# Kernel optimization log

Hardware: AMD Instinct MI355X
Metric: run time of the kernel (lower is better)

## Reference

```python
import jax, jax.numpy as jnp
import numpy as np

N = 100000      # total nodes
E = 800000      # directed edges
DIN = 256       # input feature dim
H = 128         # hidden dim
EPS = 1e-5      # BatchNorm eps


def setup_inputs() -> dict:
    key = jax.random.key(0)
    ks = jax.random.split(key, 18)
    s = 0.05
    return {
        "x": jax.random.normal(ks[0], (N, DIN), jnp.float32),
        "src": jax.random.randint(ks[1], (E,), 0, N, dtype=jnp.int32),
        "dst": jax.random.randint(ks[2], (E,), 0, N, dtype=jnp.int32),
        "W1": jax.random.normal(ks[3], (DIN, H), jnp.float32) * s,
        "b1": jnp.zeros((H,), jnp.float32),
        "g1": jnp.ones((H,), jnp.float32),
        "be1": jnp.zeros((H,), jnp.float32),
        "W2": jax.random.normal(ks[4], (H, H), jnp.float32) * s,
        "b2": jnp.zeros((H,), jnp.float32),
        "g2": jnp.ones((H,), jnp.float32),
        "be2": jnp.zeros((H,), jnp.float32),
        "W3": jax.random.normal(ks[5], (H, H), jnp.float32) * s,
        "b3": jnp.zeros((H,), jnp.float32),
        "g3": jnp.ones((H,), jnp.float32),
        "be3": jnp.zeros((H,), jnp.float32),
        "Wf": jax.random.normal(ks[6], (H, 1), jnp.float32) * s,
        "bf": jnp.zeros((1,), jnp.float32),
    }


def _gcn_conv(h, W, b, src, dst, dis):
    # GCNConv: project, then sym-normalized aggregation over edges + self-loops
    h = h @ W                                   # [N, out]
    coef = dis[src] * dis[dst]                  # [E] edge norm weights
    agg = jax.ops.segment_sum(h[src] * coef[:, None], dst, num_segments=N)
    agg = agg + h * (dis * dis)[:, None]        # self-loop term (norm = 1/deg)
    return agg + b


def _bn_relu(h, g, be):
    # BatchNorm1d in training mode (batch stats over nodes, biased variance)
    mu = jnp.mean(h, axis=0)
    var = jnp.var(h, axis=0)
    return jax.nn.relu((h - mu) * (g / jnp.sqrt(var + EPS)) + be)


def reference(x, src, dst, W1, b1, g1, be1, W2, b2, g2, be2,
              W3, b3, g3, be3, Wf, bf):
    # degree of (A + I) counted on destination nodes, edge weight 1
    deg = jax.ops.segment_sum(jnp.ones((E,), jnp.float32), dst, num_segments=N) + 1.0
    dis = jax.lax.rsqrt(deg)                    # deg >= 1, safe

    h = _bn_relu(_gcn_conv(x, W1, b1, src, dst, dis), g1, be1)
    h = _bn_relu(_gcn_conv(h, W2, b2, src, dst, dis), g2, be2)
    h = _bn_relu(_gcn_conv(h, W3, b3, src, dst, dis), g3, be3)
    return h @ Wf + bf                          # [N, 1]
```

## Files before the change

### kernel.cpp

```cpp
#include <hip/hip_runtime.h>
#include <hip/hip_bf16.h>

typedef unsigned short ushort_t;
typedef __bf16 bf16x8 __attribute__((ext_vector_type(8)));
typedef unsigned short ushort8 __attribute__((ext_vector_type(8)));
typedef unsigned short ushort4v __attribute__((ext_vector_type(4)));
typedef float f32x4 __attribute__((ext_vector_type(4)));

#define HH 128
#define EPS 1e-5f
#define STAT_SLICES 32
#define MM1_GRID 512
#define MMBN_GRID 1024

__device__ __forceinline__ float bf2f(ushort_t u) {
    unsigned v = ((unsigned)u) << 16;
    return __builtin_bit_cast(float, v);
}
__device__ __forceinline__ ushort_t f2bf(float f) {
    unsigned u = __builtin_bit_cast(unsigned, f);
    unsigned r = (u + 0x7fffu + ((u >> 16) & 1u)) >> 16;
    return (ushort_t)r;
}
__device__ __forceinline__ float cvt(const void* p, int i, int flag) {
    return flag ? bf2f(((const ushort_t*)p)[i]) : ((const float*)p)[i];
}

__global__ void preK(const int* __restrict__ dst, int* __restrict__ counts, int E,
                     const void* W1, ushort_t* Wt1, const void* W2, ushort_t* Wt2,
                     const void* W3, ushort_t* Wt3,
                     const void* g1, const void* b1, const void* b2, const void* b3,
                     const void* g2, const void* g3, const void* be1, const void* be2,
                     const void* be3, const void* Wfp, const void* bfp,
                     float* __restrict__ cvec, int histB) {
    const int bid = blockIdx.x;
    const int tid = threadIdx.x;
    const int flag = (((const ushort_t*)g1)[0] == 0x3F80) ? 1 : 0;
    if (bid < histB) {
        int e = bid * 256 + tid;
        if (e < E) atomicAdd(&counts[dst[e]], 1);
    } else if (bid < histB + 256) {
        int idx = (bid - histB) * 256 + tid;
        const void* W; ushort_t* Wt; int K;
        if (idx < 32768)      { W = W1; Wt = Wt1; K = 256; }
        else if (idx < 49152) { W = W2; Wt = Wt2; K = 128; idx -= 32768; }
        else                  { W = W3; Wt = Wt3; K = 128; idx -= 49152; }
        int k = idx >> 7, nn = idx & 127;
        Wt[nn * K + k] = flag ? ((const ushort_t*)W)[idx] : f2bf(((const float*)W)[idx]);
    } else {
        int t = tid;
        if (t < 128) {
            cvec[t]        = cvt(b1, t, flag);
            cvec[128 + t]  = cvt(b2, t, flag);
            cvec[256 + t]  = cvt(b3, t, flag);
            cvec[384 + t]  = cvt(g1, t, flag);
            cvec[512 + t]  = cvt(g2, t, flag);
            cvec[640 + t]  = cvt(g3, t, flag);
            cvec[768 + t]  = cvt(be1, t, flag);
            cvec[896 + t]  = cvt(be2, t, flag);
            cvec[1024 + t] = cvt(be3, t, flag);
            cvec[1152 + t] = cvt(Wfp, t, flag);
            if (t == 0) cvec[1280] = cvt(bfp, 0, flag);
        }
    }
}

__global__ void scanAdisK(const int* __restrict__ cnt, int* __restrict__ partial,
                          float* __restrict__ dis, int n, int nbScan) {
    __shared__ int lds[256];
    const int tid = threadIdx.x;
    if ((int)blockIdx.x < nbScan) {
        int base = blockIdx.x * 2048 + tid * 8;
        int s = 0;
#pragma unroll
        for (int j = 0; j < 8; ++j) { int idx = base + j; if (idx < n) s += cnt[idx]; }
        lds[tid] = s; __syncthreads();
        for (int off = 128; off; off >>= 1) { if (tid < off) lds[tid] += lds[tid + off]; __syncthreads(); }
        if (tid == 0) partial[blockIdx.x] = lds[0];
    } else {
        int i = (blockIdx.x - nbScan) * 256 + tid;
        if (i < n) dis[i] = rsqrtf((float)cnt[i] + 1.0f);
    }
}

__device__ __forceinline__ void scanC2Dev(int* lds, const int* __restrict__ cnt,
                                          const int* __restrict__ partial,
                                          int* __restrict__ rowptr, int n, int bid, int nb) {
    const int tid = threadIdx.x;
    int pre = 0, tot = 0;
    for (int i = 0; i < nb; ++i) { int v = partial[i]; if (i < bid) pre += v; tot += v; }
    int base = bid * 2048 + tid * 8;
    int v[8]; int s = 0;
#pragma unroll
    for (int j = 0; j < 8; ++j) { int idx = base + j; v[j] = (idx < n) ? cnt[idx] : 0; s += v[j]; }
    lds[tid] = s; __syncthreads();
    for (int off = 1; off < 256; off <<= 1) {
        int x = (tid >= off) ? lds[tid - off] : 0;
        __syncthreads();
        lds[tid] += x;
        __syncthreads();
    }
    int excl = lds[tid] - s;
    int off0 = pre + excl;
#pragma unroll
    for (int j = 0; j < 8; ++j) {
        int idx = base + j;
        if (idx < n) { rowptr[idx] = off0; off0 += v[j]; }
    }
    if (bid == 0 && tid == 0) rowptr[n] = tot;
}

__global__ void scatterK(const int* __restrict__ src, const int* __restrict__ dst,
                         const int* __restrict__ rowptr, int* __restrict__ fill,
                         const float* __restrict__ dis,
                         uint2* __restrict__ erec, int E) {
    int e = blockIdx.x * 256 + threadIdx.x;
    if (e >= E) return;
    int d = dst[e], s = src[e];
    int old = atomicSub(&fill[d], 1);
    int pos = rowptr[d] + old - 1;
    float c = dis[s] * dis[d];
    uint2 r; r.x = (unsigned)s; r.y = __builtin_bit_cast(unsigned, c);
    erec[pos] = r;
}

__global__ __launch_bounds__(256) void mm1scanCK(const void* __restrict__ x,
                                                 const ushort_t* __restrict__ Wt1,
                                                 ushort_t* __restrict__ tbuf, int n,
                                                 const ushort_t* __restrict__ flagRef,
                                                 const int* __restrict__ cnt,
                                                 const int* __restrict__ partial,
                                                 int* __restrict__ rowptr, int nbScan) {
    __shared__ char smem[65536];
    const int tid = threadIdx.x;
    if ((int)blockIdx.x < nbScan) {
        scanC2Dev((int*)smem, cnt, partial, rowptr, n, blockIdx.x, nbScan);
        return;
    }
    const int bid = blockIdx.x - nbScan;

#pragma unroll
    for (int it = 0; it < 16; ++it) {
        int idx = tid + it * 256;
        int row = idx >> 5, seg = idx & 31;
        int p = seg ^ (row & 7);
        *(uint4*)&smem[row * 512 + p * 16] = *(const uint4*)&Wt1[row * 256 + seg * 8];
    }
    __syncthreads();

    const int lane = tid & 63, wave = tid >> 6;
    const int m = lane & 15, q = lane >> 4;
    const int flag = (flagRef[0] == 0x3F80) ? 1 : 0;
    const int nTiles = (n + 63) >> 6;

    auto loadA = [&](int tile, ushort8* a) {
        int r = tile * 64 + wave * 16 + m;
        if (r >= n) r = n - 1;
        if (flag) {
            const ushort_t* p0 = (const ushort_t*)x + (size_t)r * 256 + q * 8;
#pragma unroll
            for (int s = 0; s < 8; ++s) a[s] = *(const ushort8*)(p0 + s * 32);
        } else {
            const float* p0 = (const float*)x + (size_t)r * 256 + q * 8;
#pragma unroll
            for (int s = 0; s < 8; ++s) {
                float4 f0 = *(const float4*)(p0 + s * 32);
                float4 f1 = *(const float4*)(p0 + s * 32 + 4);
                a[s][0] = f2bf(f0.x); a[s][1] = f2bf(f0.y); a[s][2] = f2bf(f0.z); a[s][3] = f2bf(f0.w);
                a[s][4] = f2bf(f1.x); a[s][5] = f2bf(f1.y); a[s][6] = f2bf(f1.z); a[s][7] = f2bf(f1.w);
            }
        }
    };

    ushort8 cur[8], nxt[8];
    int tile = bid;
    if (tile < nTiles) loadA(tile, cur);
    for (; tile < nTiles; tile += MM1_GRID) {
        int tnext = tile + MM1_GRID;
        if (tnext < nTiles) loadA(tnext, nxt);

        f32x4 acc[8];
#pragma unroll
        for (int t = 0; t < 8; ++t) acc[t] = (f32x4){0.f, 0.f, 0.f, 0.f};
#pragma unroll
        for (int s = 0; s < 8; ++s) {
            bf16x8 nf = __builtin_bit_cast(bf16x8, cur[s]);
#pragma unroll
            for (int t = 0; t < 8; ++t) {
                int p = (s * 4 + q) ^ (m & 7);
                ushort8 wv = *(const ushort8*)&smem[(t * 16 + m) * 512 + p * 16];
                acc[t] = __builtin_amdgcn_mfma_f32_16x16x32_bf16(
                    __builtin_bit_cast(bf16x8, wv), nf, acc[t], 0, 0, 0);
            }
        }
        int node_g = tile * 64 + wave * 16 + m;
        if (node_g < n) {
            ushort_t* op = tbuf + (size_t)node_g * HH + q * 4;
#pragma unroll
            for (int t = 0; t < 8; ++t) {
                ushort4v pk;
#pragma unroll
                for (int r = 0; r < 4; ++r) pk[r] = f2bf(acc[t][r]);
                *(ushort4v*)(op + t * 16) = pk;
            }
        }
#pragma unroll
        for (int s = 0; s < 8; ++s) cur[s] = nxt[s];
    }
}

__global__ __launch_bounds__(256) void mmBNK(const ushort_t* __restrict__ A,
                                             const ushort_t* __restrict__ Wt,
                                             ushort_t* __restrict__ out, int n,
                                             const float* __restrict__ ssum,
                                             const float* __restrict__ ssq,
                                             const float* __restrict__ gam,
                                             const float* __restrict__ bet) {
    __shared__ char smem[33792];
    float* scw = (float*)(smem + 32768);
    const int tid = threadIdx.x;

    if (tid < 128) {
        float S = 0.f, Q = 0.f;
#pragma unroll
        for (int sl = 0; sl < STAT_SLICES; ++sl) { S += ssum[sl * HH + tid]; Q += ssq[sl * HH + tid]; }
        float invn = 1.0f / (float)n;
        float mu = S * invn;
        float var = fmaxf(Q * invn - mu * mu, 0.f);
        float sc = gam[tid] * rsqrtf(var + EPS);
        scw[tid] = sc;
        scw[128 + tid] = bet[tid] - mu * sc;
    }
#pragma unroll
    for (int it = 0; it < 8; ++it) {
        int idx = tid + it * 256;
        int row = idx >> 4, seg = idx & 15;
        int p = seg ^ (row & 7);
        *(uint4*)&smem[row * 256 + p * 16] = *(const uint4*)&Wt[row * 128 + seg * 8];
    }
    __syncthreads();

    const int lane = tid & 63, wave = tid >> 6;
    const int m = lane & 15, q = lane >> 4;
    const int nTiles = (n + 63) >> 6;

    auto loadA = [&](int tile, ushort8* a) {
        int r = tile * 64 + wave * 16 + m;
        if (r >= n) r = n - 1;
        const ushort_t* p0 = A + (size_t)r * 128 + q * 8;
#pragma unroll
        for (int s = 0; s < 4; ++s) a[s] = *(const ushort8*)(p0 + s * 32);
    };

    ushort8 cur[4], nxt[4];
    int tile = blockIdx.x;
    if (tile < nTiles) loadA(tile, cur);
    for (; tile < nTiles; tile += MMBN_GRID) {
        int tnext = tile + MMBN_GRID;
        if (tnext < nTiles) loadA(tnext, nxt);

#pragma unroll
        for (int s = 0; s < 4; ++s) {
            int kb = s * 32 + q * 8;
#pragma unroll
            for (int j = 0; j < 8; ++j)
                cur[s][j] = f2bf(fmaxf(bf2f(cur[s][j]) * scw[kb + j] + scw[128 + kb + j], 0.f));
        }

        f32x4 acc[8];
#pragma unroll
        for (int t = 0; t < 8; ++t) acc[t] = (f32x4){0.f, 0.f, 0.f, 0.f};
#pragma unroll
        for (int s = 0; s < 4; ++s) {
            bf16x8 nf = __builtin_bit_cast(bf16x8, cur[s]);
#pragma unroll
            for (int t = 0; t < 8; ++t) {
                int p = (s * 4 + q) ^ (m & 7);
                ushort8 wv = *(const ushort8*)&smem[(t * 16 + m) * 256 + p * 16];
                acc[t] = __builtin_amdgcn_mfma_f32_16x16x32_bf16(
                    __builtin_bit_cast(bf16x8, wv), nf, acc[t], 0, 0, 0);
            }
        }
        int node_g = tile * 64 + wave * 16 + m;
        if (node_g < n) {
            ushort_t* op = out + (size_t)node_g * HH + q * 4;
#pragma unroll
            for (int t = 0; t < 8; ++t) {
                ushort4v pk;
#pragma unroll
                for (int r = 0; r < 4; ++r) pk[r] = f2bf(acc[t][r]);
                *(ushort4v*)(op + t * 16) = pk;
            }
        }
#pragma unroll
        for (int s = 0; s < 4; ++s) cur[s] = nxt[s];
    }
}

__global__ __launch_bounds__(256) void aggK(const ushort_t* __restrict__ t,
                                            const uint2* __restrict__ erec,
                                            const int* __restrict__ rowptr,
                                            const float* __restrict__ dis,
                                            const float* __restrict__ bias,
                                            ushort_t* __restrict__ g,
                                            float* __restrict__ ssum, float* __restrict__ ssq,
                                            int n) {
    const int lane = threadIdx.x & 63;
    const int wave = threadIdx.x >> 6;
    const int cb = lane * 2;
    const float b0 = bias[cb], b1 = bias[cb + 1];
    float s0 = 0.f, s1 = 0.f, q0 = 0.f, q1 = 0.f;

    for (int node = blockIdx.x * 4 + wave; node < n; node += gridDim.x * 4) {
        float d = dis[node];
        float d2 = d * d;
        unsigned sv = *(const unsigned*)(t + (size_t)node * HH + cb);
        float a0 = bf2f((ushort_t)(sv & 0xffff)) * d2;
        float a1 = bf2f((ushort_t)(sv >> 16)) * d2;

        int beg = rowptr[node], end = rowptr[node + 1];
        for (int eb = beg; eb < end; eb += 64) {
            int rem = end - eb; if (rem > 64) rem = 64;
            uint2 rec = (lane < rem) ? erec[eb + lane] : (uint2){0u, 0u};
            int es = (int)rec.x;
            float ec = __builtin_bit_cast(float, rec.y);
            int rr = (rem + 7) & ~7;
            for (int j = 0; j < rr; j += 8) {
                int ii[8]; float cc[8]; unsigned ww[8];
#pragma unroll
                for (int k = 0; k < 8; ++k) {
                    ii[k] = __shfl(es, j + k);
                    cc[k] = __shfl(ec, j + k);
                }
#pragma unroll
                for (int k = 0; k < 8; ++k)
                    ww[k] = *(const unsigned*)(t + (size_t)ii[k] * HH + cb);
#pragma unroll
                for (int k = 0; k < 8; ++k) {
                    a0 += bf2f((ushort_t)(ww[k] & 0xffff)) * cc[k];
                    a1 += bf2f((ushort_t)(ww[k] >> 16)) * cc[k];
                }
            }
        }
        a0 += b0; a1 += b1;
        unsigned packed = (unsigned)f2bf(a0) | ((unsigned)f2bf(a1) << 16);
        *(unsigned*)(g + (size_t)node * HH + cb) = packed;
        s0 += a0; s1 += a1; q0 += a0 * a0; q1 += a1 * a1;
    }

    __shared__ float red[4][64][4];
    red[wave][lane][0] = s0; red[wave][lane][1] = s1;
    red[wave][lane][2] = q0; red[wave][lane][3] = q1;
    __syncthreads();
    if (wave == 0) {
        float S0 = 0, S1 = 0, Q0 = 0, Q1 = 0;
#pragma unroll
        for (int w = 0; w < 4; ++w) {
            S0 += red[w][lane][0]; S1 += red[w][lane][1];
            Q0 += red[w][lane][2]; Q1 += red[w][lane][3];
        }
        int slice = (blockIdx.x & (STAT_SLICES - 1)) * HH;
        atomicAdd(&ssum[slice + cb], S0);
        atomicAdd(&ssum[slice + cb + 1], S1);
        atomicAdd(&ssq[slice + cb], Q0);
        atomicAdd(&ssq[slice + cb + 1], Q1);
    }
}

__global__ __launch_bounds__(256) void outK(const ushort_t* __restrict__ g,
                                            const float* __restrict__ ssum,
                                            const float* __restrict__ ssq,
                                            const float* __restrict__ gam,
                                            const float* __restrict__ bet,
                                            const float* __restrict__ Wf,
                                            const float* __restrict__ bfp,
                                            void* __restrict__ outv, int n,
                                            const ushort_t* __restrict__ flagRef) {
    __shared__ float scw[256];
    const int tid = threadIdx.x;
    if (tid < 128) {
        float S = 0.f, Q = 0.f;
#pragma unroll
        for (int sl = 0; sl < STAT_SLICES; ++sl) { S += ssum[sl * HH + tid]; Q += ssq[sl * HH + tid]; }
        float invn = 1.0f / (float)n;
        float mu = S * invn;
        float var = fmaxf(Q * invn - mu * mu, 0.f);
        float sc = gam[tid] * rsqrtf(var + EPS);
        scw[tid] = sc;
        scw[128 + tid] = bet[tid] - mu * sc;
    }
    __syncthreads();

    const int lane = tid & 63;
    const int wave = tid >> 6;
    const int cb = lane * 2;
    const float w0 = Wf[cb], w1 = Wf[cb + 1];
    const float sc0 = scw[cb], sc1 = scw[cb + 1];
    const float sh0 = scw[128 + cb], sh1 = scw[128 + cb + 1];
    const float bb = bfp[0];
    const int flag = (flagRef[0] == 0x3F80) ? 1 : 0;

    for (int node = blockIdx.x * 4 + wave; node < n; node += gridDim.x * 4) {
        unsigned v = *(const unsigned*)(g + (size_t)node * HH + cb);
        float h0 = fmaxf(bf2f((ushort_t)(v & 0xffff)) * sc0 + sh0, 0.f);
        float h1 = fmaxf(bf2f((ushort_t)(v >> 16)) * sc1 + sh1, 0.f);
        float x = h0 * w0 + h1 * w1;
#pragma unroll
        for (int off = 32; off; off >>= 1) x += __shfl_down(x, off);
        if (lane == 0) {
            float r = x + bb;
            if (flag) ((ushort_t*)outv)[node] = f2bf(r);
            else      ((float*)outv)[node] = r;
        }
    }
}

extern "C" void kernel_launch(void* const* d_in, const int* in_sizes, int n_in,
                              void* d_out, int out_size, void* d_ws, size_t ws_size,
                              hipStream_t stream) {
    const int DIN = 256;
    const int N = in_sizes[0] / DIN;
    const int E = in_sizes[1];

    const void* x   = d_in[0];
    const int*  src = (const int*)d_in[1];
    const int*  dst = (const int*)d_in[2];
    const void* W1  = d_in[3];
    const void* b1  = d_in[4];
    const void* g1  = d_in[5];
    const void* be1 = d_in[6];
    const void* W2  = d_in[7];
    const void* b2  = d_in[8];
    const void* g2  = d_in[9];
    const void* be2 = d_in[10];
    const void* W3  = d_in[11];
    const void* b3  = d_in[12];
    const void* g3  = d_in[13];
    const void* be3 = d_in[14];
    const void* Wf  = d_in[15];
    const void* bfp = d_in[16];
    const ushort_t* flagRef = (const ushort_t*)g1;

    char* base = (char*)d_ws;
    size_t off = 0;
    auto carve = [&](size_t bytes) -> void* {
        void* p = base + off;
        off += (bytes + 255) & ~(size_t)255;
        return p;
    };
    int*      counts = (int*)carve((size_t)N * 4);
    float*    stats  = (float*)carve((size_t)3 * 2 * STAT_SLICES * HH * 4);
    size_t    zbytes = off;
    float*    dis    = (float*)carve((size_t)N * 4);
    int*      rowptr = (int*)carve((size_t)(N + 1) * 4);
    int*      partial= (int*)carve(256 * 4);
    uint2*    erec   = (uint2*)carve((size_t)E * 8);
    ushort_t* Wt1    = (ushort_t*)carve((size_t)128 * 256 * 2);
    ushort_t* Wt2    = (ushort_t*)carve((size_t)128 * 128 * 2);
    ushort_t* Wt3    = (ushort_t*)carve((size_t)128 * 128 * 2);
    ushort_t* tbuf   = (ushort_t*)carve((size_t)N * HH * 2);
    ushort_t* gbuf   = (ushort_t*)carve((size_t)N * HH * 2);
    float*    cvec   = (float*)carve((size_t)1281 * 4);

    float* ssum0 = stats;                         float* ssq0 = ssum0 + STAT_SLICES * HH;
    float* ssum1 = ssq0 + STAT_SLICES * HH;       float* ssq1 = ssum1 + STAT_SLICES * HH;
    float* ssum2 = ssq1 + STAT_SLICES * HH;       float* ssq2 = ssum2 + STAT_SLICES * HH;

    float* c_b1 = cvec;         float* c_b2 = cvec + 128;  float* c_b3 = cvec + 256;
    float* c_g1 = cvec + 384;   float* c_g2 = cvec + 512;  float* c_g3 = cvec + 640;
    float* c_be1 = cvec + 768;  float* c_be2 = cvec + 896; float* c_be3 = cvec + 1024;
    float* c_Wf = cvec + 1152;  float* c_bf = cvec + 1280;

    const int nbScan = (N + 2047) / 2048;
    const int histB  = (E + 255) / 256;
    const int disB   = (N + 255) / 256;
    const int aggB   = 2048;

    hipMemsetAsync(d_ws, 0, zbytes, stream);

    preK<<<histB + 256 + 1, 256, 0, stream>>>(dst, counts, E, W1, Wt1, W2, Wt2, W3, Wt3,
                                              g1, b1, b2, b3, g2, g3, be1, be2, be3, Wf, bfp,
                                              cvec, histB);
    scanAdisK<<<nbScan + disB, 256, 0, stream>>>(counts, partial, dis, N, nbScan);
    mm1scanCK<<<nbScan + MM1_GRID, 256, 0, stream>>>(x, Wt1, tbuf, N, flagRef,
                                                     counts, partial, rowptr, nbScan);
    scatterK<<<histB, 256, 0, stream>>>(src, dst, rowptr, counts, dis, erec, E);

    aggK<<<aggB, 256, 0, stream>>>(tbuf, erec, rowptr, dis, c_b1, gbuf, ssum0, ssq0, N);
    mmBNK<<<MMBN_GRID, 256, 0, stream>>>(gbuf, Wt2, tbuf, N, ssum0, ssq0, c_g1, c_be1);
    aggK<<<aggB, 256, 0, stream>>>(tbuf, erec, rowptr, dis, c_b2, gbuf, ssum1, ssq1, N);
    mmBNK<<<MMBN_GRID, 256, 0, stream>>>(gbuf, Wt3, tbuf, N, ssum1, ssq1, c_g2, c_be2);
    aggK<<<aggB, 256, 0, stream>>>(tbuf, erec, rowptr, dis, c_b3, gbuf, ssum2, ssq2, N);
    outK<<<1024, 256, 0, stream>>>(gbuf, ssum2, ssq2, c_g3, c_be3, c_Wf, c_bf, d_out, N, flagRef);
}
```

Measured before the change: 452.9 us.

## Stage A tiles via global_load_lds DMA and split first GEMM output columns

Both GEMM kernels now copy the activation tile straight from global memory into LDS with global_load_lds, replacing register prefetch with double-buffered cur/nxt arrays. The first GEMM splits its 128 output columns into two halves across block pairs, so each block keeps half of W1 in LDS, and the fp32 input path converts rows into LDS. The mmBN grid shrinks from 1024 to 768. This removes the software prefetch overlap, so each tile waits for its DMA before the MFMAs run, and the column split makes each input tile be read twice from global memory.

```diff
diff --git a/kernel.cpp b/kernel.cpp
--- a/kernel.cpp
+++ b/kernel.cpp
@@ -10,8 +10,8 @@
 #define HH 128
 #define EPS 1e-5f
 #define STAT_SLICES 32
-#define MM1_GRID 512
-#define MMBN_GRID 1024
+#define GAS __attribute__((address_space(1)))
+#define LAS __attribute__((address_space(3)))
 
 __device__ __forceinline__ float bf2f(ushort_t u) {
     unsigned v = ((unsigned)u) << 16;
@@ -24,6 +24,9 @@
 }
 __device__ __forceinline__ float cvt(const void* p, int i, int flag) {
     return flag ? bf2f(((const ushort_t*)p)[i]) : ((const float*)p)[i];
+}
+__device__ __forceinline__ void dma16(const void* g, void* l) {
+    __builtin_amdgcn_global_load_lds((const GAS unsigned*)g, (LAS unsigned*)l, 16, 0, 0);
 }
 
 __global__ void preK(const int* __restrict__ dst, int* __restrict__ counts, int E,
@@ -134,17 +137,18 @@
     __shared__ char smem[65536];
     const int tid = threadIdx.x;
     if ((int)blockIdx.x < nbScan) {
-        scanC2Dev((int*)smem, cnt, partial, rowptr, n, blockIdx.x, nbScan);
+        scanC2Dev((int*)smem, cnt, partial, rowptr, n, blockIdx.x - 0, nbScan);
         return;
     }
-    const int bid = blockIdx.x - nbScan;
-
-#pragma unroll
-    for (int it = 0; it < 16; ++it) {
+    const int arm = blockIdx.x - nbScan;
+    const int ch  = arm & 1;
+
+#pragma unroll
+    for (int it = 0; it < 8; ++it) {
         int idx = tid + it * 256;
-        int row = idx >> 5, seg = idx & 31;
-        int p = seg ^ (row & 7);
-        *(uint4*)&smem[row * 512 + p * 16] = *(const uint4*)&Wt1[row * 256 + seg * 8];
+        int r = idx >> 5, seg = idx & 31;
+        int p = seg ^ (r & 7);
+        *(uint4*)&smem[r * 512 + p * 16] = *(const uint4*)&Wt1[(size_t)(ch * 64 + r) * 256 + seg * 8];
     }
     __syncthreads();
 
@@ -152,60 +156,62 @@
     const int m = lane & 15, q = lane >> 4;
     const int flag = (flagRef[0] == 0x3F80) ? 1 : 0;
     const int nTiles = (n + 63) >> 6;
-
-    auto loadA = [&](int tile, ushort8* a) {
-        int r = tile * 64 + wave * 16 + m;
-        if (r >= n) r = n - 1;
+    char* abuf = smem + 32768;
+
+    for (int tile = (arm >> 1); tile < nTiles; tile += 256) {
+        const int row0 = tile * 64 + wave * 16;
         if (flag) {
-            const ushort_t* p0 = (const ushort_t*)x + (size_t)r * 256 + q * 8;
-#pragma unroll
-            for (int s = 0; s < 8; ++s) a[s] = *(const ushort8*)(p0 + s * 32);
+#pragma unroll
+            for (int j = 0; j < 8; ++j) {
+                int r = row0 + j * 2;
+                if (r + 1 >= n) r = n - 2;
+                const char* g = (const char*)x + (size_t)r * 512 + lane * 16;
+                dma16(g, abuf + (wave * 16 + j * 2) * 512);
+            }
+            __builtin_amdgcn_s_waitcnt(0x0F70);
         } else {
-            const float* p0 = (const float*)x + (size_t)r * 256 + q * 8;
-#pragma unroll
-            for (int s = 0; s < 8; ++s) {
-                float4 f0 = *(const float4*)(p0 + s * 32);
-                float4 f1 = *(const float4*)(p0 + s * 32 + 4);
-                a[s][0] = f2bf(f0.x); a[s][1] = f2bf(f0.y); a[s][2] = f2bf(f0.z); a[s][3] = f2bf(f0.w);
-                a[s][4] = f2bf(f1.x); a[s][5] = f2bf(f1.y); a[s][6] = f2bf(f1.z); a[s][7] = f2bf(f1.w);
-            }
-        }
-    };
-
-    ushort8 cur[8], nxt[8];
-    int tile = bid;
-    if (tile < nTiles) loadA(tile, cur);
-    for (; tile < nTiles; tile += MM1_GRID) {
-        int tnext = tile + MM1_GRID;
-        if (tnext < nTiles) loadA(tnext, nxt);
-
-        f32x4 acc[8];
-#pragma unroll
-        for (int t = 0; t < 8; ++t) acc[t] = (f32x4){0.f, 0.f, 0.f, 0.f};
+#pragma unroll
+            for (int j = 0; j < 8; ++j) {
+                int r = row0 + j * 2;
+                if (r + 1 >= n) r = n - 2;
+                int rr = r + (lane >> 5);
+                int off = (lane & 31) * 8;
+                const float* p = (const float*)x + (size_t)rr * 256 + off;
+                float4 f0 = *(const float4*)p, f1 = *(const float4*)(p + 4);
+                ushort8 v;
+                v[0] = f2bf(f0.x); v[1] = f2bf(f0.y); v[2] = f2bf(f0.z); v[3] = f2bf(f0.w);
+                v[4] = f2bf(f1.x); v[5] = f2bf(f1.y); v[6] = f2bf(f1.z); v[7] = f2bf(f1.w);
+                *(ushort8*)&abuf[(wave * 16 + j * 2) * 512 + lane * 16] = v;
+            }
+        }
+
+        f32x4 acc[4];
+#pragma unroll
+        for (int t = 0; t < 4; ++t) acc[t] = (f32x4){0.f, 0.f, 0.f, 0.f};
+        const char* arow = abuf + (wave * 16 + m) * 512;
 #pragma unroll
         for (int s = 0; s < 8; ++s) {
-            bf16x8 nf = __builtin_bit_cast(bf16x8, cur[s]);
-#pragma unroll
-            for (int t = 0; t < 8; ++t) {
+            ushort8 av = *(const ushort8*)(arow + s * 64 + q * 16);
+            bf16x8 nf = __builtin_bit_cast(bf16x8, av);
+#pragma unroll
+            for (int t = 0; t < 4; ++t) {
                 int p = (s * 4 + q) ^ (m & 7);
                 ushort8 wv = *(const ushort8*)&smem[(t * 16 + m) * 512 + p * 16];
                 acc[t] = __builtin_amdgcn_mfma_f32_16x16x32_bf16(
                     __builtin_bit_cast(bf16x8, wv), nf, acc[t], 0, 0, 0);
             }
         }
-        int node_g = tile * 64 + wave * 16 + m;
-        if (node_g < n) {
-            ushort_t* op = tbuf + (size_t)node_g * HH + q * 4;
-#pragma unroll
-            for (int t = 0; t < 8; ++t) {
+        int node = tile * 64 + wave * 16 + m;
+        if (node < n) {
+            ushort_t* op = tbuf + (size_t)node * HH + ch * 64 + q * 4;
+#pragma unroll
+            for (int t = 0; t < 4; ++t) {
                 ushort4v pk;
 #pragma unroll
                 for (int r = 0; r < 4; ++r) pk[r] = f2bf(acc[t][r]);
                 *(ushort4v*)(op + t * 16) = pk;
             }
         }
-#pragma unroll
-        for (int s = 0; s < 8; ++s) cur[s] = nxt[s];
     }
 }
 
@@ -216,8 +222,9 @@
                                              const float* __restrict__ ssq,
                                              const float* __restrict__ gam,
                                              const float* __restrict__ bet) {
-    __shared__ char smem[33792];
-    float* scw = (float*)(smem + 32768);
+    __shared__ char smem[50176];
+    char* abuf = smem + 32768;
+    float* scw = (float*)(smem + 49152);
     const int tid = threadIdx.x;
 
     if (tid < 128) {
@@ -234,9 +241,9 @@
 #pragma unroll
     for (int it = 0; it < 8; ++it) {
         int idx = tid + it * 256;
-        int row = idx >> 4, seg = idx & 15;
-        int p = seg ^ (row & 7);
-        *(uint4*)&smem[row * 256 + p * 16] = *(const uint4*)&Wt[row * 128 + seg * 8];
+        int r = idx >> 4, seg = idx & 15;
+        int p = seg ^ (r & 7);
+        *(uint4*)&smem[r * 256 + p * 16] = *(const uint4*)&Wt[(size_t)r * 128 + seg * 8];
     }
     __syncthreads();
 
@@ -244,35 +251,29 @@
     const int m = lane & 15, q = lane >> 4;
     const int nTiles = (n + 63) >> 6;
 
-    auto loadA = [&](int tile, ushort8* a) {
-        int r = tile * 64 + wave * 16 + m;
-        if (r >= n) r = n - 1;
-        const ushort_t* p0 = A + (size_t)r * 128 + q * 8;
-#pragma unroll
-        for (int s = 0; s < 4; ++s) a[s] = *(const ushort8*)(p0 + s * 32);
-    };
-
-    ushort8 cur[4], nxt[4];
-    int tile = blockIdx.x;
-    if (tile < nTiles) loadA(tile, cur);
-    for (; tile < nTiles; tile += MMBN_GRID) {
-        int tnext = tile + MMBN_GRID;
-        if (tnext < nTiles) loadA(tnext, nxt);
-
+    for (int tile = blockIdx.x; tile < nTiles; tile += gridDim.x) {
+        const int row0 = tile * 64 + wave * 16;
+#pragma unroll
+        for (int j = 0; j < 4; ++j) {
+            int r = row0 + j * 4;
+            if (r + 3 >= n) r = n - 4;
+            const char* g = (const char*)A + (size_t)r * 256 + lane * 16;
+            dma16(g, abuf + (wave * 16 + j * 4) * 256);
+        }
+        __builtin_amdgcn_s_waitcnt(0x0F70);
+
+        f32x4 acc[8];
+#pragma unroll
+        for (int t = 0; t < 8; ++t) acc[t] = (f32x4){0.f, 0.f, 0.f, 0.f};
+        const char* arow = abuf + (wave * 16 + m) * 256;
 #pragma unroll
         for (int s = 0; s < 4; ++s) {
+            ushort8 av = *(const ushort8*)(arow + s * 64 + q * 16);
             int kb = s * 32 + q * 8;
 #pragma unroll
             for (int j = 0; j < 8; ++j)
-                cur[s][j] = f2bf(fmaxf(bf2f(cur[s][j]) * scw[kb + j] + scw[128 + kb + j], 0.f));
-        }
-
-        f32x4 acc[8];
-#pragma unroll
-        for (int t = 0; t < 8; ++t) acc[t] = (f32x4){0.f, 0.f, 0.f, 0.f};
-#pragma unroll
-        for (int s = 0; s < 4; ++s) {
-            bf16x8 nf = __builtin_bit_cast(bf16x8, cur[s]);
+                av[j] = f2bf(fmaxf(bf2f(av[j]) * scw[kb + j] + scw[128 + kb + j], 0.f));
+            bf16x8 nf = __builtin_bit_cast(bf16x8, av);
 #pragma unroll
             for (int t = 0; t < 8; ++t) {
                 int p = (s * 4 + q) ^ (m & 7);
@@ -281,9 +282,9 @@
                     __builtin_bit_cast(bf16x8, wv), nf, acc[t], 0, 0, 0);
             }
         }
-        int node_g = tile * 64 + wave * 16 + m;
-        if (node_g < n) {
-            ushort_t* op = out + (size_t)node_g * HH + q * 4;
+        int node = tile * 64 + wave * 16 + m;
+        if (node < n) {
+            ushort_t* op = out + (size_t)node * HH + q * 4;
 #pragma unroll
             for (int t = 0; t < 8; ++t) {
                 ushort4v pk;
@@ -292,8 +293,6 @@
                 *(ushort4v*)(op + t * 16) = pk;
             }
         }
-#pragma unroll
-        for (int s = 0; s < 4; ++s) cur[s] = nxt[s];
     }
 }
 
@@ -482,14 +481,14 @@
                                               g1, b1, b2, b3, g2, g3, be1, be2, be3, Wf, bfp,
                                               cvec, histB);
     scanAdisK<<<nbScan + disB, 256, 0, stream>>>(counts, partial, dis, N, nbScan);
-    mm1scanCK<<<nbScan + MM1_GRID, 256, 0, stream>>>(x, Wt1, tbuf, N, flagRef,
-                                                     counts, partial, rowptr, nbScan);
+    mm1scanCK<<<nbScan + 512, 256, 0, stream>>>(x, Wt1, tbuf, N, flagRef,
+                                                counts, partial, rowptr, nbScan);
     scatterK<<<histB, 256, 0, stream>>>(src, dst, rowptr, counts, dis, erec, E);
 
     aggK<<<aggB, 256, 0, stream>>>(tbuf, erec, rowptr, dis, c_b1, gbuf, ssum0, ssq0, N);
-    mmBNK<<<MMBN_GRID, 256, 0, stream>>>(gbuf, Wt2, tbuf, N, ssum0, ssq0, c_g1, c_be1);
+    mmBNK<<<768, 256, 0, stream>>>(gbuf, Wt2, tbuf, N, ssum0, ssq0, c_g1, c_be1);
     aggK<<<aggB, 256, 0, stream>>>(tbuf, erec, rowptr, dis, c_b2, gbuf, ssum1, ssq1, N);
-    mmBNK<<<MMBN_GRID, 256, 0, stream>>>(gbuf, Wt3, tbuf, N, ssum1, ssq1, c_g2, c_be2);
+    mmBNK<<<768, 256, 0, stream>>>(gbuf, Wt3, tbuf, N, ssum1, ssq1, c_g2, c_be2);
     aggK<<<aggB, 256, 0, stream>>>(tbuf, erec, rowptr, dis, c_b3, gbuf, ssum2, ssq2, N);
     outK<<<1024, 256, 0, stream>>>(gbuf, ssum2, ssq2, c_g3, c_be3, c_Wf, c_bf, d_out, N, flagRef);
 }
```

After: 435.7 us. -3.8%, faster.
